# Kernel tuning notes

Hardware: AMD Instinct MI355X
Metric: run time of the kernel (lower is better)

The kernel has to match this reference:

```python
import jax, jax.numpy as jnp
import numpy as np

B, C_IN, C_OUT, H, W = 128, 64, 64, 56, 56
NUM_EXPERTS = 8
N_ROUTED = NUM_EXPERTS - 1


def setup_inputs() -> dict:
    key = jax.random.key(0)
    ks = jax.random.split(key, 7)
    x = jax.random.normal(ks[0], (B, C_IN, H, W), dtype=jnp.float32)
    weights = jax.random.uniform(ks[1], (B,), dtype=jnp.float32)
    indices = jax.random.randint(ks[2], (B,), 0, N_ROUTED, dtype=jnp.int32)
    # shared expert: 1x1 conv == per-pixel linear, weight [out, in], bias [out]
    s = 1.0 / np.sqrt(C_IN)
    W_shared = jax.random.uniform(ks[3], (C_OUT, C_IN), minval=-s, maxval=s, dtype=jnp.float32)
    b_shared = jax.random.uniform(ks[4], (C_OUT,), minval=-s, maxval=s, dtype=jnp.float32)
    # routed experts stacked: [E, out, in] and [E, out]
    W_routed = jax.random.uniform(ks[5], (N_ROUTED, C_OUT, C_IN), minval=-s, maxval=s, dtype=jnp.float32)
    b_routed = jax.random.uniform(ks[6], (N_ROUTED, C_OUT), minval=-s, maxval=s, dtype=jnp.float32)
    return {"x": x, "weights": weights, "indices": indices,
            "W_shared": W_shared, "b_shared": b_shared,
            "W_routed": W_routed, "b_routed": b_routed}


def reference(x, weights, indices, W_shared, b_shared, W_routed, b_routed):
    # Shared expert (1x1 conv): [B,C_in,H,W] -> [B,C_out,H,W]
    shared = jnp.einsum('oi,bihw->bohw', W_shared, x) + b_shared[None, :, None, None]
    # Routed: each sample b uses expert indices[b]; gather per-sample expert params
    W_sel = W_routed[indices]           # [B, out, in]
    b_sel = b_routed[indices]           # [B, out]
    routed = jnp.einsum('boi,bihw->bohw', W_sel, x) + b_sel[:, :, None, None]
    routed = routed * weights[:, None, None, None]
    return shared + routed
```

## Files before the change

kernel.cpp:

```cpp
#include <hip/hip_runtime.h>
#include <stdint.h>


typedef __bf16 bf16x8 __attribute__((ext_vector_type(8)));
typedef float  f32x16 __attribute__((ext_vector_type(16)));

#define HW    3136
#define CIN   64
#define COUT  64
#define PXB   128
#define NPXB  25

__device__ __forceinline__ void g2lds16(const float* g, float* lds_base) {
    __builtin_amdgcn_global_load_lds(
        (const __attribute__((address_space(1))) void*)g,
        (__attribute__((address_space(3))) void*)lds_base,
        16, 0, 0);
}

__global__ __launch_bounds__(256, 4) void moe_mfma(
    const float* __restrict__ x,
    const float* __restrict__ weights,
    const int*   __restrict__ indices,
    const float* __restrict__ W_shared,
    const float* __restrict__ b_shared,
    const float* __restrict__ W_routed,
    const float* __restrict__ b_routed,
    float* __restrict__ out)
{
    __shared__ float xl[CIN * PXB];

    const int bs = blockIdx.y;
    int px0 = blockIdx.x * PXB;
    if (px0 > HW - PXB) px0 = HW - PXB;

    const int wave = threadIdx.x >> 6;
    const int lane = threadIdx.x & 63;
    const int l5   = lane >> 5;
    const int l31  = lane & 31;

    const float wb = weights[bs];
    const int   e  = indices[bs];

    const float* __restrict__ xs = x + (size_t)bs * CIN * HW;

    #pragma unroll
    for (int i = 0; i < 8; ++i) {
        const int row = 16 * wave + 2 * i;
        g2lds16(xs + (size_t)(row + l5) * HW + px0 + 4 * l31,
                xl + row * PXB);
    }

    const int ob = (wave >> 1) * 32;
    bf16x8 afrag[4];
    {
        const float* Ws = W_shared + (size_t)(ob + l31) * CIN + 8 * l5;
        const float* Wr = W_routed + ((size_t)e * COUT + ob + l31) * CIN + 8 * l5;
        #pragma unroll
        for (int ks = 0; ks < 4; ++ks) {
            float4 s0 = *(const float4*)(Ws + 16 * ks);
            float4 s1 = *(const float4*)(Ws + 16 * ks + 4);
            float4 r0 = *(const float4*)(Wr + 16 * ks);
            float4 r1 = *(const float4*)(Wr + 16 * ks + 4);
            afrag[ks][0] = (__bf16)(s0.x + wb * r0.x);
            afrag[ks][1] = (__bf16)(s0.y + wb * r0.y);
            afrag[ks][2] = (__bf16)(s0.z + wb * r0.z);
            afrag[ks][3] = (__bf16)(s0.w + wb * r0.w);
            afrag[ks][4] = (__bf16)(s1.x + wb * r1.x);
            afrag[ks][5] = (__bf16)(s1.y + wb * r1.y);
            afrag[ks][6] = (__bf16)(s1.z + wb * r1.z);
            afrag[ks][7] = (__bf16)(s1.w + wb * r1.w);
        }
    }
    f32x16 biasv;
    #pragma unroll
    for (int g = 0; g < 4; ++g) {
        const int o4 = ob + 8 * g + 4 * l5;
        float4 s = *(const float4*)(b_shared + o4);
        float4 r = *(const float4*)(b_routed + e * COUT + o4);
        biasv[4 * g + 0] = s.x + wb * r.x;
        biasv[4 * g + 1] = s.y + wb * r.y;
        biasv[4 * g + 2] = s.z + wb * r.z;
        biasv[4 * g + 3] = s.w + wb * r.w;
    }

    __syncthreads();

    const int pxh = (wave & 1) * 64;
    float* __restrict__ os = out + (size_t)bs * COUT * HW + px0;

    #pragma unroll
    for (int t = 0; t < 2; ++t) {
        const int pxl = pxh + 32 * t + l31;
        f32x16 acc = biasv;
        #pragma unroll
        for (int ks = 0; ks < 4; ++ks) {
            bf16x8 bfr;
            #pragma unroll
            for (int j = 0; j < 8; ++j)
                bfr[j] = (__bf16)xl[(16 * ks + 8 * l5 + j) * PXB + pxl];
            acc = __builtin_amdgcn_mfma_f32_32x32x16_bf16(afrag[ks], bfr, acc, 0, 0, 0);
        }
        #pragma unroll
        for (int r = 0; r < 16; ++r) {
            const int row = ob + (r & 3) + 8 * (r >> 2) + 4 * l5;
            os[(size_t)row * HW + pxl] = acc[r];
        }
    }
}

extern "C" void kernel_launch(void* const* d_in, const int* in_sizes, int n_in,
                              void* d_out, int out_size, void* d_ws, size_t ws_size,
                              hipStream_t stream) {
    const float* x        = (const float*)d_in[0];
    const float* weights  = (const float*)d_in[1];
    const int*   indices  = (const int*)  d_in[2];
    const float* W_shared = (const float*)d_in[3];
    const float* b_shared = (const float*)d_in[4];
    const float* W_routed = (const float*)d_in[5];
    const float* b_routed = (const float*)d_in[6];
    float* out = (float*)d_out;

    moe_mfma<<<dim3(NPXB, 128), 256, 0, stream>>>(
        x, weights, indices, W_shared, b_shared, W_routed, b_routed, out);
}
```

Baseline: 44.96 us.

## Make blocks persistent over pixel tiles with double-buffered LDS loads and shared weight staging

Each block now handles seven 64-pixel tiles of one sample instead of a single 128-pixel tile. The next tile's x is prefetched into a second LDS buffer while the current tile is computed, and the grid shrinks from 25x128 to 7x128 blocks. The combined bf16 weight is built once per block into a swizzled LDS array and read back as MFMA A fragments, which replaces redundant per-wave global loads. The exact tiling also removes the overlapping last tile. The cost is a barrier per tile and far fewer blocks (896), which may leave the GPU under-occupied and weaken latency hiding for this memory-bound kernel.

```diff
diff --git a/kernel.cpp b/kernel.cpp
--- a/kernel.cpp
+++ b/kernel.cpp
@@ -8,8 +8,9 @@
 #define HW    3136
 #define CIN   64
 #define COUT  64
-#define PXB   128
-#define NPXB  25
+#define PXB   64
+#define NT    7
+#define BPX   (PXB * NT)
 
 __device__ __forceinline__ void g2lds16(const float* g, float* lds_base) {
     __builtin_amdgcn_global_load_lds(
@@ -28,50 +29,55 @@
     const float* __restrict__ b_routed,
     float* __restrict__ out)
 {
-    __shared__ float xl[CIN * PXB];
+    __shared__ __attribute__((aligned(16))) float  xl[2][CIN * PXB];
+    __shared__ __attribute__((aligned(16))) __bf16 wl[COUT * CIN];
 
-    const int bs = blockIdx.y;
-    int px0 = blockIdx.x * PXB;
-    if (px0 > HW - PXB) px0 = HW - PXB;
+    const int bs      = blockIdx.y;
+    const int px_base = blockIdx.x * BPX;
 
-    const int wave = threadIdx.x >> 6;
-    const int lane = threadIdx.x & 63;
+    const int tid  = threadIdx.x;
+    const int wave = tid >> 6;
+    const int lane = tid & 63;
     const int l5   = lane >> 5;
     const int l31  = lane & 31;
 
     const float wb = weights[bs];
     const int   e  = indices[bs];
 
-    const float* __restrict__ xs = x + (size_t)bs * CIN * HW;
+    const float* __restrict__ xs = x   + (size_t)bs * CIN  * HW;
+    float*       __restrict__ os = out + (size_t)bs * COUT * HW;
 
-    #pragma unroll
-    for (int i = 0; i < 8; ++i) {
-        const int row = 16 * wave + 2 * i;
-        g2lds16(xs + (size_t)(row + l5) * HW + px0 + 4 * l31,
-                xl + row * PXB);
+    {
+        const float4* Ws4 = (const float4*)W_shared;
+        const float4* Wr4 = (const float4*)(W_routed + (size_t)e * (COUT * CIN));
+        #pragma unroll
+        for (int it = 0; it < 4; ++it) {
+            const int f4 = tid + it * 256;
+            float4 s = Ws4[f4], r = Wr4[f4];
+            const int o = f4 >> 4;
+            const int k = (f4 & 15) * 4;
+            __bf16* dst = (__bf16*)((char*)wl +
+                          ((((o * 64 + k) * 2)) ^ ((o & 7) << 4)));
+            dst[0] = (__bf16)(s.x + wb * r.x);
+            dst[1] = (__bf16)(s.y + wb * r.y);
+            dst[2] = (__bf16)(s.z + wb * r.z);
+            dst[3] = (__bf16)(s.w + wb * r.w);
+        }
     }
 
+    #define STAGE(BI, T) do {                                              \
+        const float* xs_t = xs + px_base + (T) * PXB;                      \
+        _Pragma("unroll")                                                  \
+        for (int i_ = 0; i_ < 4; ++i_) {                                   \
+            const int row_ = 16 * wave + 4 * i_;                           \
+            g2lds16(xs_t + (size_t)(row_ + (lane >> 4)) * HW + 4 * (lane & 15), \
+                    &xl[BI][row_ * PXB]);                                  \
+        }                                                                  \
+    } while (0)
+
+    STAGE(0, 0);
+
     const int ob = (wave >> 1) * 32;
-    bf16x8 afrag[4];
-    {
-        const float* Ws = W_shared + (size_t)(ob + l31) * CIN + 8 * l5;
-        const float* Wr = W_routed + ((size_t)e * COUT + ob + l31) * CIN + 8 * l5;
-        #pragma unroll
-        for (int ks = 0; ks < 4; ++ks) {
-            float4 s0 = *(const float4*)(Ws + 16 * ks);
-            float4 s1 = *(const float4*)(Ws + 16 * ks + 4);
-            float4 r0 = *(const float4*)(Wr + 16 * ks);
-            float4 r1 = *(const float4*)(Wr + 16 * ks + 4);
-            afrag[ks][0] = (__bf16)(s0.x + wb * r0.x);
-            afrag[ks][1] = (__bf16)(s0.y + wb * r0.y);
-            afrag[ks][2] = (__bf16)(s0.z + wb * r0.z);
-            afrag[ks][3] = (__bf16)(s0.w + wb * r0.w);
-            afrag[ks][4] = (__bf16)(s1.x + wb * r1.x);
-            afrag[ks][5] = (__bf16)(s1.y + wb * r1.y);
-            afrag[ks][6] = (__bf16)(s1.z + wb * r1.z);
-            afrag[ks][7] = (__bf16)(s1.w + wb * r1.w);
-        }
-    }
     f32x16 biasv;
     #pragma unroll
     for (int g = 0; g < 4; ++g) {
@@ -86,26 +92,42 @@
 
     __syncthreads();
 
-    const int pxh = (wave & 1) * 64;
-    float* __restrict__ os = out + (size_t)bs * COUT * HW + px0;
+    bf16x8 afrag[4];
+    {
+        const int arow = ob + l31;
+        #pragma unroll
+        for (int ks = 0; ks < 4; ++ks) {
+            const int byte = ((arow * 64 + 16 * ks + 8 * l5) * 2)
+                             ^ ((arow & 7) << 4);
+            afrag[ks] = *(const bf16x8*)((const char*)wl + byte);
+        }
+    }
 
-    #pragma unroll
-    for (int t = 0; t < 2; ++t) {
-        const int pxl = pxh + 32 * t + l31;
+    const int pxl = (wave & 1) * 32 + l31;
+
+    #pragma unroll 1
+    for (int t = 0; t < NT; ++t) {
+        if (t + 1 < NT) STAGE((t + 1) & 1, t + 1);
+
+        const float* xb = xl[t & 1];
         f32x16 acc = biasv;
         #pragma unroll
         for (int ks = 0; ks < 4; ++ks) {
             bf16x8 bfr;
             #pragma unroll
             for (int j = 0; j < 8; ++j)
-                bfr[j] = (__bf16)xl[(16 * ks + 8 * l5 + j) * PXB + pxl];
+                bfr[j] = (__bf16)xb[(16 * ks + 8 * l5 + j) * PXB + pxl];
             acc = __builtin_amdgcn_mfma_f32_32x32x16_bf16(afrag[ks], bfr, acc, 0, 0, 0);
         }
+
+        float* os_t = os + px_base + t * PXB;
         #pragma unroll
         for (int r = 0; r < 16; ++r) {
             const int row = ob + (r & 3) + 8 * (r >> 2) + 4 * l5;
-            os[(size_t)row * HW + pxl] = acc[r];
+            os_t[(size_t)row * HW + pxl] = acc[r];
         }
+
+        __syncthreads();
     }
 }
 
@@ -121,6 +143,6 @@
     const float* b_routed = (const float*)d_in[6];
     float* out = (float*)d_out;
 
-    moe_mfma<<<dim3(NPXB, 128), 256, 0, stream>>>(
+    moe_mfma<<<dim3(7, 128), 256, 0, stream>>>(
         x, weights, indices, W_shared, b_shared, W_routed, b_routed, out);
 }
```

Result: faster. 37.58 us (-16.4%).
